# Performance work log

Hardware: AMD Instinct MI355X
Metric: run time of the kernel (lower is better)

Reference implementation:

```python
import jax, jax.numpy as jnp
import numpy as np

N = 100000
E = 3200000
IN_C, HID_C, OUT_C = 128, 64, 16
NEG_SLOPE = 0.2


def setup_inputs() -> dict:
    key = jax.random.key(0)
    ks = jax.random.split(key, 12)
    x = jax.random.normal(ks[0], (N, IN_C), dtype=jnp.float32)
    # edges with no self-loops (reference then appends one self-loop per node,
    # matching add_remaining_self_loops on a loop-free graph)
    src = jax.random.randint(ks[1], (E,), 0, N)
    off = jax.random.randint(ks[2], (E,), 1, N)
    dst = (src + off) % N
    edge_index = jnp.stack([src, dst]).astype(jnp.int64)
    W1 = jax.random.normal(ks[3], (IN_C, HID_C), jnp.float32) / np.sqrt(IN_C)
    a_src1 = jax.random.normal(ks[4], (HID_C,), jnp.float32) / np.sqrt(HID_C)
    a_dst1 = jax.random.normal(ks[5], (HID_C,), jnp.float32) / np.sqrt(HID_C)
    b1 = jnp.zeros((HID_C,), jnp.float32)
    W2 = jax.random.normal(ks[6], (HID_C, OUT_C), jnp.float32) / np.sqrt(HID_C)
    a_src2 = jax.random.normal(ks[7], (OUT_C,), jnp.float32) / np.sqrt(OUT_C)
    a_dst2 = jax.random.normal(ks[8], (OUT_C,), jnp.float32) / np.sqrt(OUT_C)
    b2 = jnp.zeros((OUT_C,), jnp.float32)
    return {"x": x, "edge_index": edge_index, "W1": W1, "a_src1": a_src1,
            "a_dst1": a_dst1, "b1": b1, "W2": W2, "a_src2": a_src2,
            "a_dst2": a_dst2, "b2": b2}


def gat_conv(x, src, dst, W, a_src, a_dst, b):
    # x: [N, Cin] -> h: [N, Cout]
    h = x @ W
    # per-node attention halves, then per-edge score e_ij = LeakyReLU(a_s[src]+a_d[dst])
    s = h @ a_src  # [N]
    d = h @ a_dst  # [N]
    e = jax.nn.leaky_relu(s[src] + d[dst], NEG_SLOPE)  # [E']
    # segment softmax over incoming edges of each destination node
    m = jax.ops.segment_max(e, dst, num_segments=N)
    m = jnp.where(jnp.isfinite(m), m, 0.0)
    p = jnp.exp(e - m[dst])
    z = jax.ops.segment_sum(p, dst, num_segments=N)
    coef = p / (z[dst] + 1e-16)  # [E']
    # scatter-aggregate messages h[src] weighted by attention
    out = jax.ops.segment_sum(coef[:, None] * h[src], dst, num_segments=N)
    return out + b


def reference(x, edge_index, W1, a_src1, a_dst1, b1, W2, a_src2, a_dst2, b2):
    # add_remaining_self_loops: input graph has no self-loops, so append all N
    loop = jnp.arange(N, dtype=edge_index.dtype)
    src = jnp.concatenate([edge_index[0], loop])
    dst = jnp.concatenate([edge_index[1], loop])
    h = gat_conv(x, src, dst, W1, a_src1, a_dst1, b1)
    h = jax.nn.relu(h)  # dropout is identity at eval
    h = gat_conv(h, src, dst, W2, a_src2, a_dst2, b2)
    return jax.nn.log_softmax(h, axis=1)
```

## Files before the change

kernel.cpp:

```cpp
#include <hip/hip_runtime.h>
#include <math.h>

#define NEG 0.2f

__device__ __forceinline__ float leaky(float x){ return x >= 0.f ? x : NEG*x; }

__device__ __forceinline__ unsigned short f2b(float f){
    unsigned u = __float_as_uint(f);
    unsigned r = u + 0x7fffu + ((u >> 16) & 1u);
    return (unsigned short)(r >> 16);
}

__global__ __launch_bounds__(256) void rg1(const float* __restrict__ x,
        const float* __restrict__ W1, const float* __restrict__ a_src,
        const float* __restrict__ a_dst, unsigned short* __restrict__ h1b,
        float* __restrict__ s1, float* __restrict__ d1, int N,
        const int* __restrict__ ei, int* __restrict__ cnt,
        unsigned* __restrict__ rank32, int E, int ET)
{
    __shared__ float wsh[128][64];
    const int tid = threadIdx.x;
    int i0 = (blockIdx.x*256 + tid)*4;
    if (i0 < ET){
        unsigned pk;
        if (i0 + 3 < E){
            int4 d4 = *(const int4*)(ei + E + i0);
            unsigned r0 = (unsigned)atomicAdd(&cnt[d4.x], 1);
            unsigned r1 = (unsigned)atomicAdd(&cnt[d4.y], 1);
            unsigned r2 = (unsigned)atomicAdd(&cnt[d4.z], 1);
            unsigned r3 = (unsigned)atomicAdd(&cnt[d4.w], 1);
            pk = (r0 & 255u) | ((r1 & 255u) << 8) | ((r2 & 255u) << 16) | ((r3 & 255u) << 24);
        } else {
            pk = 0u;
            #pragma unroll
            for (int u = 0; u < 4; ++u){
                int i = i0 + u;
                if (i < ET){
                    int dst = (i < E) ? ei[E + i] : (i - E);
                    pk |= ((unsigned)atomicAdd(&cnt[dst], 1) & 255u) << (u*8);
                }
            }
        }
        rank32[i0 >> 2] = pk;
    }
    const int gG1 = (N + 63) >> 6;
    if ((int)blockIdx.x >= gG1) return;
    const int rowbase = blockIdx.x * 64;
    #pragma unroll
    for (int i = 0; i < 8; ++i){
        int g = tid + i*256;
        ((float4*)&wsh[0][0])[g] = ((const float4*)W1)[g];
    }
    __syncthreads();
    const int tx = tid & 15, ty = tid >> 4;
    const int r0 = rowbase + ty*4;
    const float4* xr0 = (const float4*)(x + (size_t)min(r0+0, N-1)*128);
    const float4* xr1 = (const float4*)(x + (size_t)min(r0+1, N-1)*128);
    const float4* xr2 = (const float4*)(x + (size_t)min(r0+2, N-1)*128);
    const float4* xr3 = (const float4*)(x + (size_t)min(r0+3, N-1)*128);
    float acc[4][4];
    #pragma unroll
    for (int j=0;j<4;++j){
        #pragma unroll
        for (int c=0;c<4;++c) acc[j][c]=0.f;
    }
    #pragma unroll 4
    for (int k4 = 0; k4 < 32; ++k4){
        float4 xv[4], wv[4];
        xv[0] = xr0[k4]; xv[1] = xr1[k4]; xv[2] = xr2[k4]; xv[3] = xr3[k4];
        #pragma unroll
        for (int i=0;i<4;++i) wv[i] = *(const float4*)&wsh[k4*4+i][tx*4];
        #pragma unroll
        for (int j=0;j<4;++j){
            float x0=xv[j].x, x1=xv[j].y, x2=xv[j].z, x3=xv[j].w;
            acc[j][0]=fmaf(x0,wv[0].x,acc[j][0]); acc[j][1]=fmaf(x0,wv[0].y,acc[j][1]);
            acc[j][2]=fmaf(x0,wv[0].z,acc[j][2]); acc[j][3]=fmaf(x0,wv[0].w,acc[j][3]);
            acc[j][0]=fmaf(x1,wv[1].x,acc[j][0]); acc[j][1]=fmaf(x1,wv[1].y,acc[j][1]);
            acc[j][2]=fmaf(x1,wv[1].z,acc[j][2]); acc[j][3]=fmaf(x1,wv[1].w,acc[j][3]);
            acc[j][0]=fmaf(x2,wv[2].x,acc[j][0]); acc[j][1]=fmaf(x2,wv[2].y,acc[j][1]);
            acc[j][2]=fmaf(x2,wv[2].z,acc[j][2]); acc[j][3]=fmaf(x2,wv[2].w,acc[j][3]);
            acc[j][0]=fmaf(x3,wv[3].x,acc[j][0]); acc[j][1]=fmaf(x3,wv[3].y,acc[j][1]);
            acc[j][2]=fmaf(x3,wv[3].z,acc[j][2]); acc[j][3]=fmaf(x3,wv[3].w,acc[j][3]);
        }
    }
    const float4 asv = *(const float4*)&a_src[tx*4];
    const float4 adv = *(const float4*)&a_dst[tx*4];
    #pragma unroll
    for (int j=0;j<4;++j){
        int r = rowbase + ty*4 + j;
        float sv = acc[j][0]*asv.x + acc[j][1]*asv.y + acc[j][2]*asv.z + acc[j][3]*asv.w;
        float dv = acc[j][0]*adv.x + acc[j][1]*adv.y + acc[j][2]*adv.z + acc[j][3]*adv.w;
        #pragma unroll
        for (int dd=8; dd>0; dd>>=1){ sv += __shfl_xor(sv, dd, 16); dv += __shfl_xor(dv, dd, 16); }
        if (r < N){
            uint2 pk;
            pk.x = (unsigned)f2b(acc[j][0]) | ((unsigned)f2b(acc[j][1]) << 16);
            pk.y = (unsigned)f2b(acc[j][2]) | ((unsigned)f2b(acc[j][3]) << 16);
            *(uint2*)&h1b[(size_t)r*64 + tx*4] = pk;
            if (tx == 0){ s1[r] = sv; d1[r] = dv; }
        }
    }
}

__global__ void k_scan1(const int* __restrict__ cnt, int* __restrict__ bsum, int n){
    __shared__ int sh[256];
    int b = blockIdx.x, tid = threadIdx.x;
    int start = b*1024, s = 0;
    for (int i = tid; i < 1024; i += 256){ int idx = start+i; s += (idx<n)?cnt[idx]:0; }
    sh[tid]=s; __syncthreads();
    for (int d=128; d>0; d>>=1){ if (tid<d) sh[tid]+=sh[tid+d]; __syncthreads(); }
    if (tid==0) bsum[b]=sh[0];
}
__global__ void k_scan3(const int* __restrict__ cnt, const int* __restrict__ bsum,
                        int* __restrict__ rowptr, int n){
    __shared__ int sh[256];
    __shared__ int basesh;
    int b = blockIdx.x, tid = threadIdx.x;
    int pb = 0;
    for (int i = tid; i < b; i += 256) pb += bsum[i];
    sh[tid] = pb; __syncthreads();
    for (int d=128; d>0; d>>=1){ if (tid<d) sh[tid]+=sh[tid+d]; __syncthreads(); }
    if (tid==0) basesh = sh[0];
    __syncthreads();
    int base = basesh;
    __syncthreads();
    int i0 = b*1024 + tid*4;
    int v[4]; int local=0;
    #pragma unroll
    for (int k=0;k<4;k++){ int idx=i0+k; v[k]=(idx<n)?cnt[idx]:0; local+=v[k]; }
    sh[tid]=local; __syncthreads();
    for (int d=1; d<256; d<<=1){
        int t = (tid>=d)? sh[tid-d] : 0;
        __syncthreads();
        sh[tid] += t;
        __syncthreads();
    }
    int off = base + sh[tid] - local;
    #pragma unroll
    for (int k=0;k<4;k++){
        int idx = i0+k;
        if (idx < n){
            rowptr[idx]=off; off += v[k];
            if (idx==n-1) rowptr[n]=off;
        }
    }
}

__global__ void k_score(const int* __restrict__ ei, const unsigned* __restrict__ rank32,
                        const int* __restrict__ rowptr,
                        const float* __restrict__ s, const float* __restrict__ d,
                        int2* __restrict__ csrp, int E, int ET){
    int i = blockIdx.x*256 + threadIdx.x;
    if (i >= ET) return;
    int src = (i < E) ? ei[i]     : (i - E);
    int dst = (i < E) ? ei[E + i] : (i - E);
    int lr = (int)((rank32[i >> 2] >> ((i & 3)*8)) & 255u);
    float pv = expf(leaky(s[src] + d[dst]));
    csrp[rowptr[dst] + lr] = make_int2(src, __float_as_int(pv));
}

__global__ __launch_bounds__(256) void a1(const int* __restrict__ rowptr,
        const int2* __restrict__ csrp, const unsigned short* __restrict__ h1b,
        const float* __restrict__ b1, const float* __restrict__ W2,
        const float* __restrict__ as2, const float* __restrict__ ad2,
        unsigned short* __restrict__ h2b, float* __restrict__ s2,
        float* __restrict__ d2, int N)
{
    int wid = threadIdx.x>>6, lane = threadIdx.x&63;
    int es = lane >> 3, cg = lane & 7;
    float2 w2r[8];
    #pragma unroll
    for (int j = 0; j < 8; ++j)
        w2r[j] = *(const float2*)&W2[(cg*8 + j)*16 + es*2];
    const float2 asv = *(const float2*)&as2[es*2];
    const float2 adv = *(const float2*)&ad2[es*2];
    int n = blockIdx.x*4 + wid;
    if (n >= N) return;
    int base = rowptr[n], end = rowptr[n+1];
    float a0=0.f,a1v=0.f,a2v=0.f,a3=0.f,a4=0.f,a5=0.f,a6=0.f,a7=0.f;
    float z = 0.f;
    for (int k = base + es; k < end; k += 8){
        int2 cp = csrp[k];
        float pv = __int_as_float(cp.y);
        z += pv;
        uint4 hv = *(const uint4*)(h1b + (size_t)cp.x*64 + cg*8);
        a0 = fmaf(pv, __uint_as_float(hv.x << 16),          a0);
        a1v= fmaf(pv, __uint_as_float(hv.x & 0xffff0000u),  a1v);
        a2v= fmaf(pv, __uint_as_float(hv.y << 16),          a2v);
        a3 = fmaf(pv, __uint_as_float(hv.y & 0xffff0000u),  a3);
        a4 = fmaf(pv, __uint_as_float(hv.z << 16),          a4);
        a5 = fmaf(pv, __uint_as_float(hv.z & 0xffff0000u),  a5);
        a6 = fmaf(pv, __uint_as_float(hv.w << 16),          a6);
        a7 = fmaf(pv, __uint_as_float(hv.w & 0xffff0000u),  a7);
    }
    #pragma unroll
    for (int m = 8; m <= 32; m <<= 1){
        a0 += __shfl_xor(a0, m); a1v += __shfl_xor(a1v, m);
        a2v += __shfl_xor(a2v, m); a3 += __shfl_xor(a3, m);
        a4 += __shfl_xor(a4, m); a5 += __shfl_xor(a5, m);
        a6 += __shfl_xor(a6, m); a7 += __shfl_xor(a7, m);
        z  += __shfl_xor(z, m);
    }
    float zi = 1.f/(z + 1e-16f);
    const float4 b0 = *(const float4*)(b1 + cg*8);
    const float4 b4 = *(const float4*)(b1 + cg*8 + 4);
    float o[8];
    o[0]=fmaxf(a0*zi + b0.x, 0.f); o[1]=fmaxf(a1v*zi + b0.y, 0.f);
    o[2]=fmaxf(a2v*zi + b0.z, 0.f); o[3]=fmaxf(a3*zi + b0.w, 0.f);
    o[4]=fmaxf(a4*zi + b4.x, 0.f); o[5]=fmaxf(a5*zi + b4.y, 0.f);
    o[6]=fmaxf(a6*zi + b4.z, 0.f); o[7]=fmaxf(a7*zi + b4.w, 0.f);
    float pc0 = 0.f, pc1 = 0.f;
    #pragma unroll
    for (int j = 0; j < 8; ++j){
        pc0 = fmaf(o[j], w2r[j].x, pc0);
        pc1 = fmaf(o[j], w2r[j].y, pc1);
    }
    #pragma unroll
    for (int m = 1; m <= 4; m <<= 1){ pc0 += __shfl_xor(pc0, m); pc1 += __shfl_xor(pc1, m); }
    float sp = pc0*asv.x + pc1*asv.y;
    float dp = pc0*adv.x + pc1*adv.y;
    #pragma unroll
    for (int m = 8; m <= 32; m <<= 1){ sp += __shfl_xor(sp, m); dp += __shfl_xor(dp, m); }
    if (cg == 0){
        unsigned pk = (unsigned)f2b(pc0) | ((unsigned)f2b(pc1) << 16);
        *(unsigned*)&h2b[(size_t)n*16 + es*2] = pk;
        if (es == 0){ s2[n] = sp; d2[n] = dp; }
    }
}

__global__ __launch_bounds__(256) void a2(const int* __restrict__ rowptr,
        const int2* __restrict__ csrp, const unsigned short* __restrict__ h2b,
        const float* __restrict__ s2, const float* __restrict__ d2,
        const float* __restrict__ b2, float* __restrict__ out, int N)
{
    int wid = threadIdx.x>>6, lane = threadIdx.x&63;
    int n = blockIdx.x*4 + wid;
    if (n >= N) return;
    int base = rowptr[n], end = rowptr[n+1];
    int es = lane >> 1, cg = lane & 1;
    float dn = d2[n];
    float a[8] = {0.f,0.f,0.f,0.f,0.f,0.f,0.f,0.f};
    float z = 0.f;
    for (int k = base + es; k < end; k += 32){
        int2 cp = csrp[k];
        float pv = expf(leaky(s2[cp.x] + dn));
        z += pv;
        uint4 hv = *(const uint4*)(h2b + (size_t)cp.x*16 + cg*8);
        a[0] = fmaf(pv, __uint_as_float(hv.x << 16),          a[0]);
        a[1] = fmaf(pv, __uint_as_float(hv.x & 0xffff0000u),  a[1]);
        a[2] = fmaf(pv, __uint_as_float(hv.y << 16),          a[2]);
        a[3] = fmaf(pv, __uint_as_float(hv.y & 0xffff0000u),  a[3]);
        a[4] = fmaf(pv, __uint_as_float(hv.z << 16),          a[4]);
        a[5] = fmaf(pv, __uint_as_float(hv.z & 0xffff0000u),  a[5]);
        a[6] = fmaf(pv, __uint_as_float(hv.w << 16),          a[6]);
        a[7] = fmaf(pv, __uint_as_float(hv.w & 0xffff0000u),  a[7]);
    }
    #pragma unroll
    for (int m = 2; m <= 32; m <<= 1){
        #pragma unroll
        for (int j = 0; j < 8; ++j) a[j] += __shfl_xor(a[j], m);
        z += __shfl_xor(z, m);
    }
    float zi = 1.f/(z + 1e-16f);
    const float4 b0 = *(const float4*)(b2 + cg*8);
    const float4 b4 = *(const float4*)(b2 + cg*8 + 4);
    float o[8];
    o[0]=a[0]*zi+b0.x; o[1]=a[1]*zi+b0.y; o[2]=a[2]*zi+b0.z; o[3]=a[3]*zi+b0.w;
    o[4]=a[4]*zi+b4.x; o[5]=a[5]*zi+b4.y; o[6]=a[6]*zi+b4.z; o[7]=a[7]*zi+b4.w;
    float mx = o[0];
    #pragma unroll
    for (int j = 1; j < 8; ++j) mx = fmaxf(mx, o[j]);
    mx = fmaxf(mx, __shfl_xor(mx, 1));
    float sum = 0.f;
    #pragma unroll
    for (int j = 0; j < 8; ++j) sum += expf(o[j] - mx);
    sum += __shfl_xor(sum, 1);
    if (es == 0){
        float ls = logf(sum);
        float* op = out + (size_t)n*16 + cg*8;
        *(float4*)op     = make_float4(o[0]-mx-ls, o[1]-mx-ls, o[2]-mx-ls, o[3]-mx-ls);
        *(float4*)(op+4) = make_float4(o[4]-mx-ls, o[5]-mx-ls, o[6]-mx-ls, o[7]-mx-ls);
    }
}

extern "C" void kernel_launch(void* const* d_in, const int* in_sizes, int n_in,
                              void* d_out, int out_size, void* d_ws, size_t ws_size,
                              hipStream_t stream)
{
    const float* x      = (const float*)d_in[0];
    const int*   ei     = (const int*)d_in[1];
    const float* W1     = (const float*)d_in[2];
    const float* a_src1 = (const float*)d_in[3];
    const float* a_dst1 = (const float*)d_in[4];
    const float* b1     = (const float*)d_in[5];
    const float* W2     = (const float*)d_in[6];
    const float* a_src2 = (const float*)d_in[7];
    const float* a_dst2 = (const float*)d_in[8];
    const float* b2     = (const float*)d_in[9];
    float* out = (float*)d_out;
    const int N  = in_sizes[0] / 128;
    const int E  = in_sizes[1] / 2;
    const int ET = E + N;

    char* ptr = (char*)d_ws;
    auto alloc = [&](size_t bytes)->char* {
        char* r = ptr; ptr += (bytes + 255) & ~(size_t)255; return r;
    };
    unsigned short* h1b    = (unsigned short*)alloc((size_t)N*64*2);
    unsigned short* h2b    = (unsigned short*)alloc((size_t)N*16*2);
    float*          s1     = (float*)alloc((size_t)N*4);
    float*          d1     = (float*)alloc((size_t)N*4);
    float*          s2     = (float*)alloc((size_t)N*4);
    float*          d2v    = (float*)alloc((size_t)N*4);
    int*            cnt    = (int*)alloc((size_t)N*4);
    int*            rowptr = (int*)alloc((size_t)(N+1)*4);
    unsigned*       rank32 = (unsigned*)alloc((size_t)((ET+3)/4)*4);
    int2*           csrp   = (int2*)alloc((size_t)ET*8);
    int*            bsum   = (int*)alloc(4096);

    const int gET  = (ET + 255)/256;
    const int gET4 = ((ET+3)/4 + 255)/256;
    const int nb1  = (N + 1023)/1024;
    const int nbN4 = (N + 3)/4;
    const int gG1  = (N + 63)/64;
    const int gRG1 = (gET4 > gG1) ? gET4 : gG1;

    hipMemsetAsync(cnt, 0, (size_t)N*4, stream);
    rg1<<<gRG1, 256, 0, stream>>>(x, W1, a_src1, a_dst1, h1b, s1, d1, N,
                                  ei, cnt, rank32, E, ET);
    k_scan1<<<nb1, 256, 0, stream>>>(cnt, bsum, N);
    k_scan3<<<nb1, 256, 0, stream>>>(cnt, bsum, rowptr, N);

    k_score<<<gET, 256, 0, stream>>>(ei, rank32, rowptr, s1, d1, csrp, E, ET);
    a1<<<nbN4, 256, 0, stream>>>(rowptr, csrp, h1b, b1, W2, a_src2, a_dst2,
                                 h2b, s2, d2v, N);

    a2<<<nbN4, 256, 0, stream>>>(rowptr, csrp, h2b, s2, d2v, b2, out, N);
}
```

Before: 412.3 us.

## Pack CSR entries into 32 bits and drop self-loop atomics and scan kernel

Each CSR edge record is packed into one 32-bit word: a 17-bit source index plus the 15 high bits of the bf16 attention weight, replacing the 8-byte int2. Self-loops no longer go through atomic counting. Their count is added in the scan, and they are written to the last slot of each row. The two-pass scan is merged into one kernel that re-sums the preceding counts per block. This cuts CSR write and read traffic and atomic work, but stores the attention weight at reduced precision (sign bit dropped, which is safe because exp is positive), assumes N fits in 17 bits, and adds redundant prefix summation.

```diff
diff --git a/kernel.cpp b/kernel.cpp
--- a/kernel.cpp
+++ b/kernel.cpp
@@ -16,12 +16,12 @@
         const float* __restrict__ a_dst, unsigned short* __restrict__ h1b,
         float* __restrict__ s1, float* __restrict__ d1, int N,
         const int* __restrict__ ei, int* __restrict__ cnt,
-        unsigned* __restrict__ rank32, int E, int ET)
+        unsigned* __restrict__ rank32, int E)
 {
     __shared__ float wsh[128][64];
     const int tid = threadIdx.x;
     int i0 = (blockIdx.x*256 + tid)*4;
-    if (i0 < ET){
+    if (i0 < E){
         unsigned pk;
         if (i0 + 3 < E){
             int4 d4 = *(const int4*)(ei + E + i0);
@@ -35,8 +35,8 @@
             #pragma unroll
             for (int u = 0; u < 4; ++u){
                 int i = i0 + u;
-                if (i < ET){
-                    int dst = (i < E) ? ei[E + i] : (i - E);
+                if (i < E){
+                    int dst = ei[E + i];
                     pk |= ((unsigned)atomicAdd(&cnt[dst], 1) & 255u) << (u*8);
                 }
             }
@@ -102,32 +102,23 @@
     }
 }
 
-__global__ void k_scan1(const int* __restrict__ cnt, int* __restrict__ bsum, int n){
-    __shared__ int sh[256];
-    int b = blockIdx.x, tid = threadIdx.x;
-    int start = b*1024, s = 0;
-    for (int i = tid; i < 1024; i += 256){ int idx = start+i; s += (idx<n)?cnt[idx]:0; }
-    sh[tid]=s; __syncthreads();
-    for (int d=128; d>0; d>>=1){ if (tid<d) sh[tid]+=sh[tid+d]; __syncthreads(); }
-    if (tid==0) bsum[b]=sh[0];
-}
-__global__ void k_scan3(const int* __restrict__ cnt, const int* __restrict__ bsum,
-                        int* __restrict__ rowptr, int n){
+__global__ void k_scan(const int* __restrict__ cnt, int* __restrict__ rowptr, int n){
     __shared__ int sh[256];
     __shared__ int basesh;
     int b = blockIdx.x, tid = threadIdx.x;
+    int lim = b*1024;
     int pb = 0;
-    for (int i = tid; i < b; i += 256) pb += bsum[i];
+    for (int i = tid; i < lim; i += 256) pb += cnt[i];
     sh[tid] = pb; __syncthreads();
     for (int d=128; d>0; d>>=1){ if (tid<d) sh[tid]+=sh[tid+d]; __syncthreads(); }
-    if (tid==0) basesh = sh[0];
+    if (tid==0) basesh = sh[0] + lim;
     __syncthreads();
     int base = basesh;
     __syncthreads();
     int i0 = b*1024 + tid*4;
     int v[4]; int local=0;
     #pragma unroll
-    for (int k=0;k<4;k++){ int idx=i0+k; v[k]=(idx<n)?cnt[idx]:0; local+=v[k]; }
+    for (int k=0;k<4;k++){ int idx=i0+k; v[k]=(idx<n)?(cnt[idx]+1):0; local+=v[k]; }
     sh[tid]=local; __syncthreads();
     for (int d=1; d<256; d<<=1){
         int t = (tid>=d)? sh[tid-d] : 0;
@@ -149,18 +140,24 @@
 __global__ void k_score(const int* __restrict__ ei, const unsigned* __restrict__ rank32,
                         const int* __restrict__ rowptr,
                         const float* __restrict__ s, const float* __restrict__ d,
-                        int2* __restrict__ csrp, int E, int ET){
+                        unsigned* __restrict__ csr4, int E, int ET){
     int i = blockIdx.x*256 + threadIdx.x;
     if (i >= ET) return;
-    int src = (i < E) ? ei[i]     : (i - E);
-    int dst = (i < E) ? ei[E + i] : (i - E);
-    int lr = (int)((rank32[i >> 2] >> ((i & 3)*8)) & 255u);
-    float pv = expf(leaky(s[src] + d[dst]));
-    csrp[rowptr[dst] + lr] = make_int2(src, __float_as_int(pv));
+    if (i < E){
+        int src = ei[i];
+        int dst = ei[E + i];
+        int lr = (int)((rank32[i >> 2] >> ((i & 3)*8)) & 255u);
+        float pv = expf(leaky(s[src] + d[dst]));
+        csr4[rowptr[dst] + lr] = ((unsigned)f2b(pv) << 17) | (unsigned)src;
+    } else {
+        int nn = i - E;
+        float pv = expf(leaky(s[nn] + d[nn]));
+        csr4[rowptr[nn+1] - 1] = ((unsigned)f2b(pv) << 17) | (unsigned)nn;
+    }
 }
 
 __global__ __launch_bounds__(256) void a1(const int* __restrict__ rowptr,
-        const int2* __restrict__ csrp, const unsigned short* __restrict__ h1b,
+        const unsigned* __restrict__ csr4, const unsigned short* __restrict__ h1b,
         const float* __restrict__ b1, const float* __restrict__ W2,
         const float* __restrict__ as2, const float* __restrict__ ad2,
         unsigned short* __restrict__ h2b, float* __restrict__ s2,
@@ -180,10 +177,11 @@
     float a0=0.f,a1v=0.f,a2v=0.f,a3=0.f,a4=0.f,a5=0.f,a6=0.f,a7=0.f;
     float z = 0.f;
     for (int k = base + es; k < end; k += 8){
-        int2 cp = csrp[k];
-        float pv = __int_as_float(cp.y);
+        unsigned cp = csr4[k];
+        float pv = __uint_as_float((cp >> 17) << 16);
+        int src = (int)(cp & 0x1FFFFu);
         z += pv;
-        uint4 hv = *(const uint4*)(h1b + (size_t)cp.x*64 + cg*8);
+        uint4 hv = *(const uint4*)(h1b + (size_t)src*64 + cg*8);
         a0 = fmaf(pv, __uint_as_float(hv.x << 16),          a0);
         a1v= fmaf(pv, __uint_as_float(hv.x & 0xffff0000u),  a1v);
         a2v= fmaf(pv, __uint_as_float(hv.y << 16),          a2v);
@@ -229,7 +227,7 @@
 }
 
 __global__ __launch_bounds__(256) void a2(const int* __restrict__ rowptr,
-        const int2* __restrict__ csrp, const unsigned short* __restrict__ h2b,
+        const unsigned* __restrict__ csr4, const unsigned short* __restrict__ h2b,
         const float* __restrict__ s2, const float* __restrict__ d2,
         const float* __restrict__ b2, float* __restrict__ out, int N)
 {
@@ -242,10 +240,11 @@
     float a[8] = {0.f,0.f,0.f,0.f,0.f,0.f,0.f,0.f};
     float z = 0.f;
     for (int k = base + es; k < end; k += 32){
-        int2 cp = csrp[k];
-        float pv = expf(leaky(s2[cp.x] + dn));
+        unsigned cp = csr4[k];
+        int src = (int)(cp & 0x1FFFFu);
+        float pv = expf(leaky(s2[src] + dn));
         z += pv;
-        uint4 hv = *(const uint4*)(h2b + (size_t)cp.x*16 + cg*8);
+        uint4 hv = *(const uint4*)(h2b + (size_t)src*16 + cg*8);
         a[0] = fmaf(pv, __uint_as_float(hv.x << 16),          a[0]);
         a[1] = fmaf(pv, __uint_as_float(hv.x & 0xffff0000u),  a[1]);
         a[2] = fmaf(pv, __uint_as_float(hv.y << 16),          a[2]);
@@ -314,26 +313,24 @@
     float*          d2v    = (float*)alloc((size_t)N*4);
     int*            cnt    = (int*)alloc((size_t)N*4);
     int*            rowptr = (int*)alloc((size_t)(N+1)*4);
-    unsigned*       rank32 = (unsigned*)alloc((size_t)((ET+3)/4)*4);
-    int2*           csrp   = (int2*)alloc((size_t)ET*8);
-    int*            bsum   = (int*)alloc(4096);
-
+    unsigned*       rank32 = (unsigned*)alloc((size_t)((E+3)/4)*4);
+    unsigned*       csr4   = (unsigned*)alloc((size_t)ET*4);
+    
     const int gET  = (ET + 255)/256;
-    const int gET4 = ((ET+3)/4 + 255)/256;
+    const int gE4  = ((E+3)/4 + 255)/256;
     const int nb1  = (N + 1023)/1024;
     const int nbN4 = (N + 3)/4;
     const int gG1  = (N + 63)/64;
-    const int gRG1 = (gET4 > gG1) ? gET4 : gG1;
+    const int gRG1 = (gE4 > gG1) ? gE4 : gG1;
 
     hipMemsetAsync(cnt, 0, (size_t)N*4, stream);
     rg1<<<gRG1, 256, 0, stream>>>(x, W1, a_src1, a_dst1, h1b, s1, d1, N,
-                                  ei, cnt, rank32, E, ET);
-    k_scan1<<<nb1, 256, 0, stream>>>(cnt, bsum, N);
-    k_scan3<<<nb1, 256, 0, stream>>>(cnt, bsum, rowptr, N);
-
-    k_score<<<gET, 256, 0, stream>>>(ei, rank32, rowptr, s1, d1, csrp, E, ET);
-    a1<<<nbN4, 256, 0, stream>>>(rowptr, csrp, h1b, b1, W2, a_src2, a_dst2,
+                                  ei, cnt, rank32, E);
+    k_scan<<<nb1, 256, 0, stream>>>(cnt, rowptr, N);
+
+    k_score<<<gET, 256, 0, stream>>>(ei, rank32, rowptr, s1, d1, csr4, E, ET);
+    a1<<<nbN4, 256, 0, stream>>>(rowptr, csr4, h1b, b1, W2, a_src2, a_dst2,
                                  h2b, s2, d2v, N);
 
-    a2<<<nbN4, 256, 0, stream>>>(rowptr, csrp, h2b, s2, d2v, b2, out, N);
-}
+    a2<<<nbN4, 256, 0, stream>>>(rowptr, csr4, h2b, s2, d2v, b2, out, N);
+}
```

Result: slower. 452.9 us (+9.9%).
